# Kernel optimization log

Measured on AMD Instinct MI355X. Metric: run time of the kernel, lower is better.

## Reference

```python
import jax, jax.numpy as jnp
import numpy as np

NUM_CLASSES = 81
THRESH_HI = 0.5
THRESH_LO = 0.4
GAMMA = 2.0
ALPHA = 0.25
VARIANCE = (0.1, 0.2)  # cfg['variance'] in ssd.pytorch
B, P, T = 32, 24564, 20


def setup_inputs() -> dict:
    key = jax.random.key(0)
    k1, k2, k3, k4, k5, k6, k7 = jax.random.split(key, 7)
    loc_data = jax.random.normal(k1, (B, P, 4), jnp.float32)
    conf_data = jax.random.normal(k2, (B, P, NUM_CLASSES), jnp.float32)
    # priors in center form (cx, cy, w, h), all in [0,1]
    pcxy = jax.random.uniform(k3, (P, 2), minval=0.05, maxval=0.95)
    pwh = jax.random.uniform(k4, (P, 2), minval=0.04, maxval=0.5)
    priors = jnp.concatenate([pcxy, pwh], axis=-1).astype(jnp.float32)
    # ground-truth boxes in point form (xmin, ymin, xmax, ymax) + label
    tcxy = jax.random.uniform(k5, (B, T, 2), minval=0.1, maxval=0.9)
    twh = jax.random.uniform(k6, (B, T, 2), minval=0.05, maxval=0.4)
    boxes = jnp.clip(jnp.concatenate([tcxy - twh / 2, tcxy + twh / 2], -1), 0.0, 1.0)
    labels = jax.random.randint(k7, (B, T), 0, NUM_CLASSES - 1).astype(jnp.float32)
    targets = jnp.concatenate([boxes, labels[..., None]], axis=-1)  # [B,T,5]
    return {"loc_data": loc_data, "conf_data": conf_data, "priors": priors, "targets": targets}


def point_form(pr):
    # center form -> (xmin,ymin,xmax,ymax)
    return jnp.concatenate([pr[:, :2] - pr[:, 2:] / 2, pr[:, :2] + pr[:, 2:] / 2], -1)


def jaccard(box_a, box_b):
    # box_a [T,4], box_b [P,4], both point form -> IoU [T,P]
    lt = jnp.maximum(box_a[:, None, :2], box_b[None, :, :2])
    rb = jnp.minimum(box_a[:, None, 2:], box_b[None, :, 2:])
    wh = jnp.clip(rb - lt, 0.0)
    inter = wh[..., 0] * wh[..., 1]
    area_a = ((box_a[:, 2] - box_a[:, 0]) * (box_a[:, 3] - box_a[:, 1]))[:, None]
    area_b = ((box_b[:, 2] - box_b[:, 0]) * (box_b[:, 3] - box_b[:, 1]))[None, :]
    return inter / (area_a + area_b - inter)


def encode(matched, priors):
    # matched [P,4] point form, priors [P,4] center form
    g_cxcy = ((matched[:, :2] + matched[:, 2:]) / 2 - priors[:, :2]) / (VARIANCE[0] * priors[:, 2:])
    g_wh = jnp.log((matched[:, 2:] - matched[:, :2]) / priors[:, 2:]) / VARIANCE[1]
    return jnp.concatenate([g_cxcy, g_wh], -1)


def match_one(truths, labels, priors):
    # truths [T,4] point form, labels [T], priors [P,4] center form
    ov = jaccard(truths, point_form(priors))          # [T,P]
    best_prior_idx = jnp.argmax(ov, axis=1)           # [T] best prior per gt
    best_truth_overlap = jnp.max(ov, axis=0)          # [P]
    best_truth_idx = jnp.argmax(ov, axis=0)           # [P]
    # ensure every gt box keeps its best prior
    best_truth_overlap = best_truth_overlap.at[best_prior_idx].set(2.0)
    best_truth_idx = best_truth_idx.at[best_prior_idx].set(jnp.arange(truths.shape[0]))
    matched = truths[best_truth_idx]                  # [P,4]
    conf = labels[best_truth_idx].astype(jnp.int32) + 1
    conf = jnp.where(best_truth_overlap < THRESH_HI, -1, conf)  # ignore band
    conf = jnp.where(best_truth_overlap < THRESH_LO, 0, conf)   # background
    return encode(matched, priors), conf


def reference(loc_data, conf_data, priors, targets):
    truths = targets[..., :4]
    labels = targets[..., 4]
    loc_t, conf_t = jax.vmap(lambda t, l: match_one(t, l, priors))(truths, labels)
    pos = conf_t > 0                                  # [B,P]
    # smooth L1 over positive priors (sum reduction)
    diff = loc_data - loc_t
    ad = jnp.abs(diff)
    sl1 = jnp.where(ad < 1.0, 0.5 * diff * diff, ad - 0.5)
    loss_l = jnp.sum(sl1 * pos[..., None])
    # focal loss over ALL locations (ignore conf==-1)
    logits = conf_data.reshape(-1, NUM_CLASSES)
    tgt = conf_t.reshape(-1)
    valid = tgt >= 0
    tgt_safe = jnp.where(valid, tgt, 0)
    logpt = jnp.take_along_axis(jax.nn.log_softmax(logits, -1), tgt_safe[:, None], 1)[:, 0]
    pt = jnp.exp(logpt)
    alpha_t = jnp.where(tgt > 0, ALPHA, 1.0 - ALPHA)
    fl = -alpha_t * (1.0 - pt) ** GAMMA * logpt
    loss_c = jnp.sum(jnp.where(valid, fl, 0.0))
    n = jnp.sum(pos).astype(loc_data.dtype)
    return loss_l / n, loss_c / n
```

## Files before the change

### kernel.cpp

```cpp
#include <hip/hip_runtime.h>

#define NCLS 81
#define BB 32
#define PP 24564
#define TT 20
#define KM_BLOCKS_X 96
#define KL_BLOCKS 2048
#define KL_ROWS 128
#define KL_CHUNKS ((BB * PP) / KL_ROWS)
#define KL_F4 ((KL_ROWS * NCLS) / 4)

__device__ __forceinline__ float iou_rn(float tx1, float ty1, float tx2, float ty2, float ta,
                                        float X1, float Y1, float X2, float Y2, float pa)
{
    float lx = fmaxf(tx1, X1);
    float ly = fmaxf(ty1, Y1);
    float rx = fminf(tx2, X2);
    float ry = fminf(ty2, Y2);
    float w = fmaxf(__fsub_rn(rx, lx), 0.0f);
    float h = fmaxf(__fsub_rn(ry, ly), 0.0f);
    float inter = __fmul_rn(w, h);
    float denom = __fsub_rn(__fadd_rn(ta, pa), inter);
    return __fdiv_rn(inter, denom);
}

__global__ __launch_bounds__(1024)
void k_best_prior(const float* __restrict__ priors,
                  const float* __restrict__ targets,
                  unsigned long long* __restrict__ bp)
{
    const int t = blockIdx.x;
    const int b = blockIdx.y;
    const float* tb = targets + (b * TT + t) * 5;
    const float tx1 = tb[0], ty1 = tb[1], tx2 = tb[2], ty2 = tb[3];
    const float ta = __fmul_rn(__fsub_rn(tx2, tx1), __fsub_rn(ty2, ty1));

    unsigned long long best = 0ull;
    for (int p = threadIdx.x; p < PP; p += 1024) {
        float px = priors[p * 4 + 0], py = priors[p * 4 + 1];
        float pw = priors[p * 4 + 2], ph = priors[p * 4 + 3];
        float hw = __fmul_rn(pw, 0.5f), hh = __fmul_rn(ph, 0.5f);
        float X1 = __fsub_rn(px, hw), Y1 = __fsub_rn(py, hh);
        float X2 = __fadd_rn(px, hw), Y2 = __fadd_rn(py, hh);
        float pa = __fmul_rn(__fsub_rn(X2, X1), __fsub_rn(Y2, Y1));
        float ov = iou_rn(tx1, ty1, tx2, ty2, ta, X1, Y1, X2, Y2, pa);
        unsigned long long pk = ((unsigned long long)__float_as_uint(ov) << 32)
                              | (unsigned long long)(0xFFFFFFFFu - (unsigned)p);
        if (pk > best) best = pk;
    }

    __shared__ unsigned long long red[1024];
    red[threadIdx.x] = best;
    __syncthreads();
    for (int s = 512; s > 0; s >>= 1) {
        if (threadIdx.x < s) {
            if (red[threadIdx.x + s] > red[threadIdx.x]) red[threadIdx.x] = red[threadIdx.x + s];
        }
        __syncthreads();
    }
    if (threadIdx.x == 0) bp[b * TT + t] = red[0];
}

__global__ __launch_bounds__(256)
void k_match(const float* __restrict__ loc,
             const float* __restrict__ priors,
             const float* __restrict__ targets,
             const unsigned long long* __restrict__ bp,
             unsigned char* __restrict__ code,
             float* __restrict__ pl, float* __restrict__ pn)
{
    const int b = blockIdx.y;
    const int p = blockIdx.x * 256 + threadIdx.x;

    __shared__ float trb[TT * 5];
    __shared__ unsigned int bpb[TT];
    if (threadIdx.x < TT * 5) trb[threadIdx.x] = targets[b * TT * 5 + threadIdx.x];
    if (threadIdx.x < TT)
        bpb[threadIdx.x] = 0xFFFFFFFFu - (unsigned)(bp[b * TT + threadIdx.x] & 0xFFFFFFFFull);
    __syncthreads();

    float accL = 0.0f, accN = 0.0f;

    if (p < PP) {
        float px = priors[p * 4 + 0], py = priors[p * 4 + 1];
        float pw = priors[p * 4 + 2], ph = priors[p * 4 + 3];
        float hw = __fmul_rn(pw, 0.5f), hh = __fmul_rn(ph, 0.5f);
        float X1 = __fsub_rn(px, hw), Y1 = __fsub_rn(py, hh);
        float X2 = __fadd_rn(px, hw), Y2 = __fadd_rn(py, hh);
        float pa = __fmul_rn(__fsub_rn(X2, X1), __fsub_rn(Y2, Y1));

        float bov = -1.0f;
        int bt = 0;
        #pragma unroll
        for (int t = 0; t < TT; ++t) {
            float tx1 = trb[t * 5 + 0], ty1 = trb[t * 5 + 1];
            float tx2 = trb[t * 5 + 2], ty2 = trb[t * 5 + 3];
            float ta2 = __fmul_rn(__fsub_rn(tx2, tx1), __fsub_rn(ty2, ty1));
            float ov = iou_rn(tx1, ty1, tx2, ty2, ta2, X1, Y1, X2, Y2, pa);
            if (ov > bov) { bov = ov; bt = t; }
        }
        bool forced = false;
        #pragma unroll
        for (int t = 0; t < TT; ++t) {
            if (bpb[t] == (unsigned)p) { bt = t; forced = true; }
        }
        if (forced) bov = 2.0f;

        int c = (int)trb[bt * 5 + 4] + 1;
        if (bov < 0.5f) c = -1;
        if (bov < 0.4f) c = 0;

        const int r = b * PP + p;
        code[r] = (unsigned char)(c + 1);

        if (c > 0) {
            float mx1 = trb[bt * 5 + 0], my1 = trb[bt * 5 + 1];
            float mx2 = trb[bt * 5 + 2], my2 = trb[bt * 5 + 3];
            float cx = __fmul_rn(__fadd_rn(mx1, mx2), 0.5f);
            float cy = __fmul_rn(__fadd_rn(my1, my2), 0.5f);
            float gx = __fdiv_rn(__fsub_rn(cx, px), __fmul_rn(0.1f, pw));
            float gy = __fdiv_rn(__fsub_rn(cy, py), __fmul_rn(0.1f, ph));
            float gw = __fdiv_rn(logf(__fdiv_rn(__fsub_rn(mx2, mx1), pw)), 0.2f);
            float gh = __fdiv_rn(logf(__fdiv_rn(__fsub_rn(my2, my1), ph)), 0.2f);
            const float* ld = loc + (size_t)r * 4;
            float g0 = ld[0] - gx, g1 = ld[1] - gy, g2 = ld[2] - gw, g3 = ld[3] - gh;
            float a0 = fabsf(g0), a1 = fabsf(g1), a2 = fabsf(g2), a3 = fabsf(g3);
            accL += (a0 < 1.0f) ? 0.5f * g0 * g0 : (a0 - 0.5f);
            accL += (a1 < 1.0f) ? 0.5f * g1 * g1 : (a1 - 0.5f);
            accL += (a2 < 1.0f) ? 0.5f * g2 * g2 : (a2 - 0.5f);
            accL += (a3 < 1.0f) ? 0.5f * g3 * g3 : (a3 - 0.5f);
            accN += 1.0f;
        }
    }

    __shared__ float red[256];
    red[threadIdx.x] = accL;
    __syncthreads();
    for (int s = 128; s; s >>= 1) {
        if (threadIdx.x < s) red[threadIdx.x] += red[threadIdx.x + s];
        __syncthreads();
    }
    if (threadIdx.x == 0) pl[blockIdx.y * KM_BLOCKS_X + blockIdx.x] = red[0];
    __syncthreads();

    red[threadIdx.x] = accN;
    __syncthreads();
    for (int s = 128; s; s >>= 1) {
        if (threadIdx.x < s) red[threadIdx.x] += red[threadIdx.x + s];
        __syncthreads();
    }
    if (threadIdx.x == 0) pn[blockIdx.y * KM_BLOCKS_X + blockIdx.x] = red[0];
}

__global__ __launch_bounds__(256)
void k_loss(const float* __restrict__ conf,
            const unsigned char* __restrict__ code,
            float* __restrict__ pc)
{
    __shared__ float buf[KL_ROWS * NCLS];

    const int tid = threadIdx.x;
    const int rl = tid >> 1;
    const int half = tid & 1;
    const int base = half ? 41 : 0;

    float accC = 0.0f;

    for (int chunk = blockIdx.x; chunk < KL_CHUNKS; chunk += KL_BLOCKS) {
        const float4* src = (const float4*)conf + (size_t)chunk * KL_F4;
        float4* dst = (float4*)buf;
        #pragma unroll
        for (int i = 0; i < 10; ++i) dst[tid + i * 256] = src[tid + i * 256];
        if (tid < KL_F4 - 2560) dst[2560 + tid] = src[2560 + tid];
        __syncthreads();

        const float* row = buf + rl * NCLS;
        float se = 0.0f;
        #pragma unroll 8
        for (int i = 0; i < 40; ++i) se += __expf(row[base + i]);
        if (!half) se += __expf(row[40]);
        se += __shfl_xor(se, 1);

        if (!half) {
            int r = chunk * KL_ROWS + rl;
            int c = (int)code[r] - 1;
            if (c >= 0) {
                float xt = row[c];
                float logpt = xt - __logf(se);
                float pt = __expf(logpt);
                float at = (c > 0) ? 0.25f : 0.75f;
                float om = 1.0f - pt;
                accC -= at * om * om * logpt;
            }
        }
        __syncthreads();
    }

    __shared__ float red[256];
    red[tid] = accC;
    __syncthreads();
    for (int s = 128; s; s >>= 1) {
        if (tid < s) red[tid] += red[tid + s];
        __syncthreads();
    }
    if (tid == 0) pc[blockIdx.x] = red[0];
}

__global__ __launch_bounds__(256)
void k_final(const float* __restrict__ pl, const float* __restrict__ pn,
             const float* __restrict__ pc, float* __restrict__ out)
{
    __shared__ float sl[256], sc[256], sn[256];
    float L = 0.0f, C = 0.0f, N = 0.0f;
    for (int i = threadIdx.x; i < BB * KM_BLOCKS_X; i += 256) { L += pl[i]; N += pn[i]; }
    for (int i = threadIdx.x; i < KL_BLOCKS; i += 256) C += pc[i];
    sl[threadIdx.x] = L; sc[threadIdx.x] = C; sn[threadIdx.x] = N;
    __syncthreads();
    for (int s = 128; s; s >>= 1) {
        if (threadIdx.x < s) {
            sl[threadIdx.x] += sl[threadIdx.x + s];
            sc[threadIdx.x] += sc[threadIdx.x + s];
            sn[threadIdx.x] += sn[threadIdx.x + s];
        }
        __syncthreads();
    }
    if (threadIdx.x == 0) {
        out[0] = sl[0] / sn[0];
        out[1] = sc[0] / sn[0];
    }
}

extern "C" void kernel_launch(void* const* d_in, const int* in_sizes, int n_in,
                              void* d_out, int out_size, void* d_ws, size_t ws_size,
                              hipStream_t stream)
{
    const float* loc     = (const float*)d_in[0];
    const float* conf    = (const float*)d_in[1];
    const float* priors  = (const float*)d_in[2];
    const float* targets = (const float*)d_in[3];
    float* out = (float*)d_out;

    char* ws = (char*)d_ws;
    unsigned long long* bp = (unsigned long long*)ws;
    unsigned char* code = (unsigned char*)(ws + 4096);
    float* pl = (float*)(ws + 4096 + 790528);
    float* pn = pl + BB * KM_BLOCKS_X;
    float* pc = pn + BB * KM_BLOCKS_X;

    k_best_prior<<<dim3(TT, BB), 1024, 0, stream>>>(priors, targets, bp);
    k_match<<<dim3(KM_BLOCKS_X, BB), 256, 0, stream>>>(loc, priors, targets, bp, code, pl, pn);
    k_loss<<<KL_BLOCKS, 256, 0, stream>>>(conf, code, pc);
    k_final<<<1, 256, 0, stream>>>(pl, pn, pc, out);
}
```

Baseline: 86.69 us.

## Double-buffer conf loads via registers, wave-shuffle reductions, division-free argmax

New measurement: 153.1 us. 1.77x slower.

```diff
diff --git a/kernel.cpp b/kernel.cpp
--- a/kernel.cpp
+++ b/kernel.cpp
@@ -6,7 +6,7 @@
 #define TT 20
 #define KM_BLOCKS_X 96
 #define KL_BLOCKS 2048
-#define KL_ROWS 128
+#define KL_ROWS 64
 #define KL_CHUNKS ((BB * PP) / KL_ROWS)
 #define KL_F4 ((KL_ROWS * NCLS) / 4)
 
@@ -49,16 +49,20 @@
         if (pk > best) best = pk;
     }
 
-    __shared__ unsigned long long red[1024];
-    red[threadIdx.x] = best;
-    __syncthreads();
-    for (int s = 512; s > 0; s >>= 1) {
-        if (threadIdx.x < s) {
-            if (red[threadIdx.x + s] > red[threadIdx.x]) red[threadIdx.x] = red[threadIdx.x + s];
-        }
-        __syncthreads();
-    }
-    if (threadIdx.x == 0) bp[b * TT + t] = red[0];
+    #pragma unroll
+    for (int s = 32; s; s >>= 1) {
+        unsigned long long o = __shfl_xor(best, s, 64);
+        if (o > best) best = o;
+    }
+    __shared__ unsigned long long wred[16];
+    if ((threadIdx.x & 63) == 0) wred[threadIdx.x >> 6] = best;
+    __syncthreads();
+    if (threadIdx.x == 0) {
+        unsigned long long b2 = wred[0];
+        #pragma unroll
+        for (int w = 1; w < 16; ++w) if (wred[w] > b2) b2 = wred[w];
+        bp[b * TT + t] = b2;
+    }
 }
 
 __global__ __launch_bounds__(256)
@@ -89,16 +93,23 @@
         float X2 = __fadd_rn(px, hw), Y2 = __fadd_rn(py, hh);
         float pa = __fmul_rn(__fsub_rn(X2, X1), __fsub_rn(Y2, Y1));
 
-        float bov = -1.0f;
+        float bI = -1.0f, bD = 1.0f;
         int bt = 0;
         #pragma unroll
         for (int t = 0; t < TT; ++t) {
             float tx1 = trb[t * 5 + 0], ty1 = trb[t * 5 + 1];
             float tx2 = trb[t * 5 + 2], ty2 = trb[t * 5 + 3];
             float ta2 = __fmul_rn(__fsub_rn(tx2, tx1), __fsub_rn(ty2, ty1));
-            float ov = iou_rn(tx1, ty1, tx2, ty2, ta2, X1, Y1, X2, Y2, pa);
-            if (ov > bov) { bov = ov; bt = t; }
-        }
+            float lx = fmaxf(tx1, X1), ly = fmaxf(ty1, Y1);
+            float rx = fminf(tx2, X2), ry = fminf(ty2, Y2);
+            float w = fmaxf(__fsub_rn(rx, lx), 0.0f);
+            float h = fmaxf(__fsub_rn(ry, ly), 0.0f);
+            float inter = __fmul_rn(w, h);
+            float denom = __fsub_rn(__fadd_rn(ta2, pa), inter);
+            if (__fmul_rn(inter, bD) > __fmul_rn(bI, denom)) { bI = inter; bD = denom; bt = t; }
+        }
+        float bov = __fdiv_rn(bI, bD);
+
         bool forced = false;
         #pragma unroll
         for (int t = 0; t < TT; ++t) {
@@ -157,43 +168,75 @@
             const unsigned char* __restrict__ code,
             float* __restrict__ pc)
 {
-    __shared__ float buf[KL_ROWS * NCLS];
+    __shared__ float buf[2][KL_ROWS * NCLS];
 
     const int tid = threadIdx.x;
-    const int rl = tid >> 1;
-    const int half = tid & 1;
-    const int base = half ? 41 : 0;
+    const int rl = tid >> 2;
+    const int k = tid & 3;
+    const float4* conf4 = (const float4*)conf;
+
+    float4 rg[6];
+
+    const int c0 = blockIdx.x;
+    {
+        const float4* src = conf4 + (size_t)c0 * KL_F4;
+        #pragma unroll
+        for (int i = 0; i < 5; ++i) rg[i] = src[tid + i * 256];
+        if (tid < KL_F4 - 1280) rg[5] = src[1280 + tid];
+        float4* dst = (float4*)buf[0];
+        #pragma unroll
+        for (int i = 0; i < 5; ++i) dst[tid + i * 256] = rg[i];
+        if (tid < KL_F4 - 1280) dst[1280 + tid] = rg[5];
+    }
+    __syncthreads();
+    if (c0 + KL_BLOCKS < KL_CHUNKS) {
+        const float4* src = conf4 + (size_t)(c0 + KL_BLOCKS) * KL_F4;
+        #pragma unroll
+        for (int i = 0; i < 5; ++i) rg[i] = src[tid + i * 256];
+        if (tid < KL_F4 - 1280) rg[5] = src[1280 + tid];
+    }
 
     float accC = 0.0f;
-
-    for (int chunk = blockIdx.x; chunk < KL_CHUNKS; chunk += KL_BLOCKS) {
-        const float4* src = (const float4*)conf + (size_t)chunk * KL_F4;
-        float4* dst = (float4*)buf;
-        #pragma unroll
-        for (int i = 0; i < 10; ++i) dst[tid + i * 256] = src[tid + i * 256];
-        if (tid < KL_F4 - 2560) dst[2560 + tid] = src[2560 + tid];
-        __syncthreads();
-
-        const float* row = buf + rl * NCLS;
+    int cur = 0;
+
+    for (int c = c0; c < KL_CHUNKS; c += KL_BLOCKS) {
+        const float* row = buf[cur] + rl * NCLS;
         float se = 0.0f;
-        #pragma unroll 8
-        for (int i = 0; i < 40; ++i) se += __expf(row[base + i]);
-        if (!half) se += __expf(row[40]);
-        se += __shfl_xor(se, 1);
-
-        if (!half) {
-            int r = chunk * KL_ROWS + rl;
-            int c = (int)code[r] - 1;
-            if (c >= 0) {
-                float xt = row[c];
+        #pragma unroll
+        for (int i = 0; i < 20; ++i) se += __expf(row[k * 20 + i]);
+        if (k == 0) se += __expf(row[80]);
+        se += __shfl_xor(se, 1, 4);
+        se += __shfl_xor(se, 2, 4);
+
+        if (k == 0) {
+            int r = c * KL_ROWS + rl;
+            int cc = (int)code[r] - 1;
+            if (cc >= 0) {
+                float xt = row[cc];
                 float logpt = xt - __logf(se);
                 float pt = __expf(logpt);
-                float at = (c > 0) ? 0.25f : 0.75f;
+                float at = (cc > 0) ? 0.25f : 0.75f;
                 float om = 1.0f - pt;
                 accC -= at * om * om * logpt;
             }
         }
-        __syncthreads();
+
+        int cnext = c + KL_BLOCKS;
+        if (cnext < KL_CHUNKS) {
+            float4* dst = (float4*)buf[cur ^ 1];
+            #pragma unroll
+            for (int i = 0; i < 5; ++i) dst[tid + i * 256] = rg[i];
+            if (tid < KL_F4 - 1280) dst[1280 + tid] = rg[5];
+            __syncthreads();
+            int c2 = cnext + KL_BLOCKS;
+            if (c2 < KL_CHUNKS) {
+                const float4* src = conf4 + (size_t)c2 * KL_F4;
+                #pragma unroll
+                for (int i = 0; i < 5; ++i) rg[i] = src[tid + i * 256];
+                if (tid < KL_F4 - 1280) rg[5] = src[1280 + tid];
+            }
+            cur ^= 1;
+        }
     }
 
     __shared__ float red[256];
```
